# Kernel tuning notes

Hardware: AMD Instinct MI355X
Metric: run time of the kernel (lower is better)

## Reference

```python
import jax, jax.numpy as jnp
import numpy as np
import math

N = 16384
IRREPS_IN = ((16, 0), (8, 1), (8, 2))          # 16x0e + 8x1e + 8x2e, dim 80
HID1 = ((128, 0), (128, 1), (128, 2), (128, 1))  # hidden_irreps[1]
HID0 = ((64, 0), (64, 1), (64, 2), (64, 1))      # hidden_irreps[0]
IRREPS_OUT = ((1, 0), (1, 2))                   # 1x0e + 1x2e, dim 6
UVU_INS = ((0,0,0),(0,1,1),(0,2,2),(0,3,3),(1,0,1),(1,1,0),(1,1,1),(1,1,3),
           (2,0,2),(2,1,2),(2,2,0),(2,2,1),(2,2,3),(2,3,2))
# FullyConnectedTensorProduct: all symmetry-allowed paths, 17 total
FC_INS = tuple((i1, i2, io) for io, (mo, lo) in enumerate(IRREPS_OUT)
               for i1, (m1, l1) in enumerate(HID0)
               for i2, (m2, l2) in enumerate(HID0)
               if abs(l1 - l2) <= lo <= l1 + l2)

# ---- real Clebsch-Gordan coefficients (computed once in numpy) ----
def _cg_complex(l1, l2, l3):
    f = math.factorial
    C = np.zeros((2*l1+1, 2*l2+1, 2*l3+1))
    for m1 in range(-l1, l1+1):
        for m2 in range(-l2, l2+1):
            m3 = m1 + m2
            if abs(m3) > l3:
                continue
            pref = math.sqrt((2*l3+1) * f(l3+l1-l2) * f(l3-l1+l2) * f(l1+l2-l3) / f(l1+l2+l3+1))
            pref *= math.sqrt(f(l3+m3)*f(l3-m3)*f(l1-m1)*f(l1+m1)*f(l2-m2)*f(l2+m2))
            s = 0.0
            for k in range(l1+l2-l3+1):
                d = (k, l1+l2-l3-k, l1-m1-k, l2+m2-k, l3-l2+m1+k, l3-l1-m2+k)
                if min(d) < 0:
                    continue
                s += (-1)**k / (f(d[0])*f(d[1])*f(d[2])*f(d[3])*f(d[4])*f(d[5]))
            C[m1+l1, m2+l2, m3+l3] = pref * s
    return C

def _real_to_complex(l):
    U = np.zeros((2*l+1, 2*l+1), dtype=complex)
    U[l, l] = 1.0
    for m in range(1, l+1):
        U[l-m, l+m] = 1/math.sqrt(2)
        U[l+m, l+m] = (-1)**m/math.sqrt(2)
        U[l-m, l-m] = 1j/math.sqrt(2)
        U[l+m, l-m] = -1j*(-1)**m/math.sqrt(2)
    return U * (-1j)**l  # phase makes the real-basis CG real

def _real_cg(l1, l2, l3):
    K = np.einsum('ma,nb,oc,mno->abc', _real_to_complex(l1), _real_to_complex(l2),
                  np.conj(_real_to_complex(l3)), _cg_complex(l1, l2, l3))
    Kr, Ki = np.real(K), np.imag(K)
    K = Kr if np.linalg.norm(Kr) >= np.linalg.norm(Ki) else Ki
    # component normalization: ||K||_F = sqrt(2*l3+1)
    return (K / np.linalg.norm(K) * math.sqrt(2*l3+1)).astype(np.float32)

_CG = {}
def cg(l1, l2, l3):
    if (l1, l2, l3) not in _CG:
        _CG[(l1, l2, l3)] = _real_cg(l1, l2, l3)
    return _CG[(l1, l2, l3)]

# ---- irreps helpers ----
def to_blocks(x, irr):
    blocks, off = [], 0
    for m, l in irr:
        d = m * (2*l + 1)
        blocks.append(x[:, off:off+d].reshape(x.shape[0], m, 2*l + 1))
        off += d
    return blocks

def from_blocks(bl):
    return jnp.concatenate([b.reshape(b.shape[0], -1) for b in bl], axis=-1)

def o3_linear(xb, irr_in, irr_out, W, b0):
    # e3nn o3.Linear: mixes all input blocks with the same l; fan-in normalized; bias on 0e
    xin = {}
    for blk, (m, l) in zip(xb, irr_in):
        xin[l] = blk if l not in xin else jnp.concatenate([xin[l], blk], axis=1)
    out, cur, boff = [], {}, 0
    for m, l in irr_out:
        c = cur.get(l, 0)
        Wl = W[l][:, c:c+m]  # (tot_in_mul_l, m)
        y = jnp.einsum('nui,uo->noi', xin[l], Wl) / np.float32(math.sqrt(xin[l].shape[1]))
        cur[l] = c + m
        if l == 0:
            y = y + b0[boff:boff+m][None, :, None]
            boff += m
        out.append(y)
    return out

def tp_uvu(x1, x2, w, irr, ins):
    # o3.TensorProduct with 'uvu' weighted paths; weight per path: (u, v)
    ls = [l for _, l in irr]
    fan = [0.0] * len(irr)
    for i1, i2, io in ins:
        fan[io] += irr[i2][0]
    out = [None] * len(irr)
    for p, (i1, i2, io) in enumerate(ins):
        K = cg(ls[i1], ls[i2], ls[io])  # (i, j, k)
        b = jnp.einsum('uv,nvj->nuj', w[p], x2[i2])
        t = jnp.einsum('nui,nuj,ijk->nuk', x1[i1], b, K)
        out[io] = t if out[io] is None else out[io] + t
    return [o / np.float32(math.sqrt(f)) for o, f in zip(out, fan)]

def tp_fc(x1, x2, w):
    ls = [l for _, l in HID0]
    fan = [0.0, 0.0]
    for i1, i2, io in FC_INS:
        fan[io] += HID0[i1][0] * HID0[i2][0]
    out = [None, None]
    for p, (i1, i2, io) in enumerate(FC_INS):
        K = cg(ls[i1], ls[i2], IRREPS_OUT[io][1])
        b = jnp.einsum('uv,nvj->nuj', w[p], x2[i2])
        t = jnp.einsum('nui,nuj,ijk->nk', x1[i1], b, K)
        out[io] = t if out[io] is None else out[io] + t
    return [(o / np.float32(math.sqrt(f)))[:, None, :] for o, f in zip(out, fan)]

def setup_inputs() -> dict:
    key = jax.random.key(0)
    ks = jax.random.split(key, 16)
    rn = lambda k, shp: jax.random.normal(k, shp, dtype=jnp.float32)
    return {
        'x': rn(ks[0], (N, 80)),
        'lin1_W0': rn(ks[1], (16, 128)), 'lin1_W1': rn(ks[2], (8, 256)),
        'lin1_W2': rn(ks[3], (8, 128)), 'lin1_b0': rn(ks[4], (128,)),
        'lin2_W0': rn(ks[5], (128, 64)), 'lin2_W1': rn(ks[6], (256, 128)),
        'lin2_W2': rn(ks[7], (128, 64)), 'lin2_b0': rn(ks[8], (64,)),
        # 11 stacked HID0->HID0 linears: [s1a, s1b, lin3, s2a, s2b, lin4, s3a, s3b, lin5, s4a, s4b]
        'L_W0': rn(ks[9], (11, 64, 64)), 'L_W1': rn(ks[10], (11, 128, 128)),
        'L_W2': rn(ks[11], (11, 64, 64)), 'L_b0': rn(ks[12], (11, 64)),
        'tp_w': rn(ks[13], (3, 14, 64, 64)),  # tp1..tp3 path weights
        'tp4_w': rn(ks[14], (17, 64, 64)),    # fully-connected tp path weights
    }

def reference(x, lin1_W0, lin1_W1, lin1_W2, lin1_b0,
              lin2_W0, lin2_W1, lin2_W2, lin2_b0,
              L_W0, L_W1, L_W2, L_b0, tp_w, tp4_w):
    h = o3_linear(to_blocks(x, IRREPS_IN), IRREPS_IN, HID1,
                  {0: lin1_W0, 1: lin1_W1, 2: lin1_W2}, lin1_b0)
    h = o3_linear(h, HID1, HID0, {0: lin2_W0, 1: lin2_W1, 2: lin2_W2}, lin2_b0)
    lin = lambda hb, i: o3_linear(hb, HID0, HID0, {0: L_W0[i], 1: L_W1[i], 2: L_W2[i]}, L_b0[i])
    for i in range(3):  # split -> tp(uvu) -> linear, three times
        ha, hb = lin(h, 3*i), lin(h, 3*i + 1)
        ht = tp_uvu(ha, hb, tp_w[i], HID0, UVU_INS)
        h = lin(ht, 3*i + 2)
    ha, hb = lin(h, 9), lin(h, 10)  # split4
    return from_blocks(tp_fc(ha, hb, tp4_w))
```

## Files before the change

kernel.cpp:

```cpp
#include <hip/hip_runtime.h>
#include <math.h>

constexpr int TS = 16;
constexpr int NT = 512;
constexpr int SSTRIDE = 776;
constexpr int H1S = 1544;
constexpr int BUF = TS*SSTRIDE;

typedef __attribute__((ext_vector_type(8))) short bf16x8;
typedef __attribute__((ext_vector_type(4))) float f32x4;
typedef __attribute__((ext_vector_type(4))) unsigned short u16x4;

#define KFENCE() asm volatile("" ::: "memory")

__device__ inline f32x4 mfma16(bf16x8 a, bf16x8 b, f32x4 c){
  return __builtin_amdgcn_mfma_f32_16x16x32_bf16(a, b, c, 0, 0, 0);
}
__device__ inline unsigned short f2b(float f){
  union { float f; unsigned u; } v; v.f = f;
  return (unsigned short)((v.u + 0x7fffu + ((v.u >> 16) & 1u)) >> 16);
}
__device__ inline float b2f(unsigned short h){
  union { unsigned u; float f; } v; v.u = ((unsigned)h) << 16; return v.f;
}
__device__ inline void store_hl(unsigned short* ph, unsigned short* pl, int idx, float v){
  unsigned short h = f2b(v);
  ph[idx] = h;
  pl[idx] = f2b(v - b2f(h));
}
#define LDFRAG(p) (*(const bf16x8*)(p))

constexpr int OFF_L2W0 = 0;
constexpr int OFF_L2W1 = 8192;
constexpr int OFF_L2W2 = 40960;
constexpr int OFF_LW0  = 49152;
constexpr int OFF_LW1  = 94208;
constexpr int OFF_LW2  = 274432;
constexpr int OFF_TPW  = 319488;
constexpr int OFF_TP4W = 491520;
constexpr int W_TOT    = 561152;

__device__ inline double dfact(int n){ double r=1.0; for(int i=2;i<=n;i++) r*=(double)i; return r; }
struct dcplx { double x, y; };
__device__ inline dcplx cmul(dcplx a, dcplx b){ return {a.x*b.x-a.y*b.y, a.x*b.y+a.y*b.x}; }

__device__ dcplx Uent(int l, int r, int c){
  double re=0.0, im=0.0;
  double s = 1.0/sqrt(2.0);
  if (r==l && c==l) re = 1.0;
  else if (c>l){ int m=c-l; double sgn=(m&1)?-1.0:1.0;
    if (r==l-m) re = s; else if (r==l+m) re = sgn*s;
  } else if (c<l){ int m=l-c; double sgn=(m&1)?-1.0:1.0;
    if (r==l-m) im = s; else if (r==l+m) im = -sgn*s;
  }
  int lm=l&3; double pr,pi;
  if(lm==0){pr=1;pi=0;} else if(lm==1){pr=0;pi=-1;} else if(lm==2){pr=-1;pi=0;} else {pr=0;pi=1;}
  return { re*pr-im*pi, re*pi+im*pr };
}

__device__ double cg_complex_entry(int l1,int l2,int l3,int m1,int m2){
  int m3=m1+m2;
  if (m3<-l3 || m3>l3) return 0.0;
  double pref = sqrt((double)(2*l3+1)*dfact(l3+l1-l2)*dfact(l3-l1+l2)*dfact(l1+l2-l3)/dfact(l1+l2+l3+1));
  pref *= sqrt(dfact(l3+m3)*dfact(l3-m3)*dfact(l1-m1)*dfact(l1+m1)*dfact(l2-m2)*dfact(l2+m2));
  double s=0.0;
  for(int k=0;k<=l1+l2-l3;k++){
    int a2=l1-m1-k, a3=l2+m2-k, a4=l3-l2+m1+k, a5=l3-l1-m2+k;
    if(a2<0||a3<0||a4<0||a5<0) continue;
    double t=1.0/(dfact(k)*dfact(l1+l2-l3-k)*dfact(a2)*dfact(a3)*dfact(a4)*dfact(a5));
    s += (k&1)? -t : t;
  }
  return pref*s;
}

__global__ void cg_init_kernel(float* cg){
  __shared__ double sKr[525], sKi[525];
  __shared__ double sScale[13];
  __shared__ int    sSel[13];
  const int L1[13]={0,0,1,0,2,1,1,1,2,1,2,2,2};
  const int L2[13]={0,1,0,2,0,1,1,1,1,2,2,2,2};
  const int L3[13]={0,1,1,2,2,0,1,2,2,2,0,1,2};
  const int OFF[14]={0,1,10,19,44,69,78,105,150,225,300,325,400,525};
  const int tid = threadIdx.x;
  int combo=-1, l1=0,l2=0,l3=0;
  if (tid < 525){
    combo=12;
    for(int i=0;i<12;i++) if (tid < OFF[i+1]) { combo=i; break; }
    l1=L1[combo]; l2=L2[combo]; l3=L3[combo];
    int d2=2*l2+1, d3=2*l3+1;
    int e = tid - OFF[combo];
    int a = e/(d2*d3), b=(e/d3)%d2, cc=e%d3;
    double kr=0.0, ki=0.0;
    for(int m=0;m<2*l1+1;m++) for(int n=0;n<d2;n++){
      int m3 = (m-l1)+(n-l2);
      if (m3<-l3||m3>l3) continue;
      double cv = cg_complex_entry(l1,l2,l3,m-l1,n-l2);
      if (cv==0.0) continue;
      dcplx u1=Uent(l1,m,a), u2=Uent(l2,n,b), u3=Uent(l3,m3+l3,cc);
      u3.y = -u3.y;
      dcplx t = cmul(cmul(u1,u2),u3);
      kr += t.x*cv; ki += t.y*cv;
    }
    sKr[tid]=kr; sKi[tid]=ki;
  }
  __syncthreads();
  if (tid < 13){
    int sz = OFF[tid+1]-OFF[tid];
    double nr=0,ni=0;
    for(int i=0;i<sz;i++){ double r=sKr[OFF[tid]+i], im=sKi[OFF[tid]+i]; nr+=r*r; ni+=im*im; }
    int sel = (nr>=ni)? 0 : 1;
    sSel[tid]=sel;
    sScale[tid] = sqrt((double)(2*L3[tid]+1))/sqrt(sel? ni : nr);
  }
  __syncthreads();
  if (tid < 525){
    double v = sSel[combo]? sKi[tid] : sKr[tid];
    cg[tid] = (float)(v*sScale[combo]);
  }
}

__global__ void prep_kernel(const float* __restrict__ l2W0, const float* __restrict__ l2W1,
                            const float* __restrict__ l2W2, const float* __restrict__ LW0,
                            const float* __restrict__ LW1, const float* __restrict__ LW2,
                            const float* __restrict__ tpw, const float* __restrict__ tp4w,
                            unsigned short* __restrict__ wb){
  int i = blockIdx.x*256 + threadIdx.x;
  if (i >= W_TOT) return;
  float v;
  if (i < 8192){ int o=i>>7, k=i&127; v = l2W0[k*64+o]; }
  else if (i < 40960){ int j=i-8192; int o=j>>8, k=j&255; v = l2W1[k*128+o]; }
  else if (i < 49152){ int j=i-40960; int o=j>>7, k=j&127; v = l2W2[k*64+o]; }
  else if (i < 94208){ int j=i-49152; int li=j>>12, r=j&4095, o=r>>6, k=r&63; v = LW0[li*4096+k*64+o]; }
  else if (i < 274432){ int j=i-94208; int li=j>>14, r=j&16383, o=r>>7, k=r&127; v = LW1[li*16384+k*128+o]; }
  else if (i < 319488){ int j=i-274432; int li=j>>12, r=j&4095, o=r>>6, k=r&63; v = LW2[li*4096+k*64+o]; }
  else if (i < 491520){ v = tpw[i-319488]; }
  else { v = tp4w[i-491520]; }
  unsigned short h = f2b(v);
  wb[i] = h;
  wb[W_TOT + i] = f2b(v - b2f(h));
}

__device__ void linL_mfma(const unsigned short* __restrict__ wb, int o0, int o1, int o2,
                          const float* __restrict__ b0,
                          const unsigned short* sh, const unsigned short* sl,
                          unsigned short* dh, unsigned short* dl, int wave, int lane)
{
  const float rs128 = 0.08838834764831845f;
  int l16 = lane & 15, quad = lane >> 4;
  int abase = l16 * SSTRIDE;
  for (int job = wave; job < 16; job += 8){
    if (job < 4){
      int col = job*16 + l16;
      f32x4 a0 = {0,0,0,0}, a1 = {0,0,0,0};
      #pragma unroll
      for (int ks=0; ks<2; ks++){
        int so = abase + ks*32 + quad*8;
        bf16x8 xh = LDFRAG(sh+so), xl = LDFRAG(sl+so);
        int wo = o0 + col*64 + ks*32 + quad*8;
        bf16x8 wh = LDFRAG(wb+wo), wl = LDFRAG(wb+W_TOT+wo);
        a0 = mfma16(xh,wh,a0); a1 = mfma16(xh,wl,a1); a1 = mfma16(xl,wh,a1);
      }
      float bias = b0[col];
      #pragma unroll
      for (int r=0;r<4;r++)
        store_hl(dh,dl,(quad*4+r)*SSTRIDE + col, (a0[r]+a1[r])*0.125f + bias);
    } else if (job < 12){
      int nt = job-4; int col = nt*16 + l16;
      #pragma unroll
      for (int i=0;i<3;i++){
        f32x4 a0 = {0,0,0,0}, a1 = {0,0,0,0};
        #pragma unroll
        for (int ks=0; ks<4; ks++){
          int ka = ks*32 + quad*8;
          int so = abase + ((ka < 64) ? (64 + i*64 + ka) : (576 + i*64 + ka - 64));
          bf16x8 xh = LDFRAG(sh+so), xl = LDFRAG(sl+so);
          int wo = o1 + col*128 + ka;
          bf16x8 wh = LDFRAG(wb+wo), wl = LDFRAG(wb+W_TOT+wo);
          a0 = mfma16(xh,wh,a0); a1 = mfma16(xh,wl,a1); a1 = mfma16(xl,wh,a1);
        }
        int dof = (col < 64) ? (64 + i*64 + col) : (576 + i*64 + col - 64);
        #pragma unroll
        for (int r=0;r<4;r++)
          store_hl(dh,dl,(quad*4+r)*SSTRIDE + dof, (a0[r]+a1[r])*rs128);
      }
    } else {
      int nt = job-12; int col = nt*16 + l16;
      #pragma unroll
      for (int i=0;i<5;i++){
        f32x4 a0 = {0,0,0,0}, a1 = {0,0,0,0};
        #pragma unroll
        for (int ks=0; ks<2; ks++){
          int so = abase + 256 + i*64 + ks*32 + quad*8;
          bf16x8 xh = LDFRAG(sh+so), xl = LDFRAG(sl+so);
          int wo = o2 + col*64 + ks*32 + quad*8;
          bf16x8 wh = LDFRAG(wb+wo), wl = LDFRAG(wb+W_TOT+wo);
          a0 = mfma16(xh,wh,a0); a1 = mfma16(xh,wl,a1); a1 = mfma16(xl,wh,a1);
        }
        #pragma unroll
        for (int r=0;r<4;r++)
          store_hl(dh,dl,(quad*4+r)*SSTRIDE + 256 + i*64 + col, (a0[r]+a1[r])*0.125f);
      }
    }
  }
}

__device__ void lin2_mfma(const unsigned short* __restrict__ wb,
                          const float* __restrict__ b0,
                          const unsigned short* h1h, const unsigned short* h1l,
                          unsigned short* dh, unsigned short* dl, int wave, int lane)
{
  const float rs128 = 0.08838834764831845f;
  int l16 = lane & 15, quad = lane >> 4;
  int abase = l16 * H1S;
  for (int job = wave; job < 16; job += 8){
    if (job < 4){
      int col = job*16 + l16;
      f32x4 a0 = {0,0,0,0}, a1 = {0,0,0,0};
      #pragma unroll
      for (int ks=0; ks<4; ks++){
        int so = abase + ks*32 + quad*8;
        bf16x8 xh = LDFRAG(h1h+so), xl = LDFRAG(h1l+so);
        int wo = OFF_L2W0 + col*128 + ks*32 + quad*8;
        bf16x8 wh = LDFRAG(wb+wo), wl = LDFRAG(wb+W_TOT+wo);
        a0 = mfma16(xh,wh,a0); a1 = mfma16(xh,wl,a1); a1 = mfma16(xl,wh,a1);
      }
      float bias = b0[col];
      #pragma unroll
      for (int r=0;r<4;r++)
        store_hl(dh,dl,(quad*4+r)*SSTRIDE + col, (a0[r]+a1[r])*rs128 + bias);
    } else if (job < 12){
      int nt = job-4; int col = nt*16 + l16;
      #pragma unroll
      for (int i=0;i<3;i++){
        f32x4 a0 = {0,0,0,0}, a1 = {0,0,0,0};
        #pragma unroll
        for (int ks=0; ks<8; ks++){
          int ka = ks*32 + quad*8;
          int so = abase + ((ka < 128) ? (128 + i*128 + ka) : (1152 + i*128 + ka - 128));
          bf16x8 xh = LDFRAG(h1h+so), xl = LDFRAG(h1l+so);
          int wo = OFF_L2W1 + col*256 + ka;
          bf16x8 wh = LDFRAG(wb+wo), wl = LDFRAG(wb+W_TOT+wo);
          a0 = mfma16(xh,wh,a0); a1 = mfma16(xh,wl,a1); a1 = mfma16(xl,wh,a1);
        }
        int dof = (col < 64) ? (64 + i*64 + col) : (576 + i*64 + col - 64);
        #pragma unroll
        for (int r=0;r<4;r++)
          store_hl(dh,dl,(quad*4+r)*SSTRIDE + dof, (a0[r]+a1[r])*0.0625f);
      }
    } else {
      int nt = job-12; int col = nt*16 + l16;
      #pragma unroll
      for (int i=0;i<5;i++){
        f32x4 a0 = {0,0,0,0}, a1 = {0,0,0,0};
        #pragma unroll
        for (int ks=0; ks<4; ks++){
          int so = abase + 512 + i*128 + ks*32 + quad*8;
          bf16x8 xh = LDFRAG(h1h+so), xl = LDFRAG(h1l+so);
          int wo = OFF_L2W2 + col*128 + ks*32 + quad*8;
          bf16x8 wh = LDFRAG(wb+wo), wl = LDFRAG(wb+W_TOT+wo);
          a0 = mfma16(xh,wh,a0); a1 = mfma16(xh,wl,a1); a1 = mfma16(xl,wh,a1);
        }
        #pragma unroll
        for (int r=0;r<4;r++)
          store_hl(dh,dl,(quad*4+r)*SSTRIDE + 256 + i*64 + col, (a0[r]+a1[r])*rs128);
      }
    }
  }
}

template<int D1,int D2,int D3,int O1,int O2,int CGO>
__device__ __forceinline__ void fused_path(
    const unsigned short* __restrict__ wb, int wo,
    const unsigned short* s1h, const unsigned short* s1l,
    const unsigned short* s2h, const unsigned short* s2l,
    const float* __restrict__ cgp,
    float (&tk)[4][D3], int mt, int lane)
{
  int l16 = lane & 15, quad = lane >> 4;
  float x1v[D1][4];
  #pragma unroll
  for (int i=0;i<D1;i++){
    int o = l16*SSTRIDE + O1 + i*64 + mt*16 + quad*4;
    u16x4 xh4 = *(const u16x4*)(s1h + o);
    u16x4 xl4 = *(const u16x4*)(s1l + o);
    #pragma unroll
    for (int r=0;r<4;r++) x1v[i][r] = b2f(xh4[r]) + b2f(xl4[r]);
  }
  #pragma unroll
  for (int j=0;j<D2;j++){
    f32x4 a0 = {0,0,0,0}, a1 = {0,0,0,0};
    #pragma unroll
    for (int ks=0; ks<2; ks++){
      int wofs = wo + (mt*16 + l16)*64 + ks*32 + quad*8;
      bf16x8 wh = LDFRAG(wb + wofs);
      bf16x8 wl = LDFRAG(wb + W_TOT + wofs);
      int sofs = l16*SSTRIDE + O2 + j*64 + ks*32 + quad*8;
      bf16x8 xh = LDFRAG(s2h + sofs);
      bf16x8 xl = LDFRAG(s2l + sofs);
      a0 = mfma16(wh,xh,a0); a1 = mfma16(wh,xl,a1); a1 = mfma16(wl,xh,a1);
    }
    #pragma unroll
    for (int r=0;r<4;r++){
      float bu = a0[r] + a1[r];
      #pragma unroll
      for (int i=0;i<D1;i++){
        float pr = x1v[i][r]*bu;
        #pragma unroll
        for (int k=0;k<D3;k++) tk[r][k] += pr*cgp[CGO + (i*D2 + j)*D3 + k];
      }
    }
  }
}

template<int D1,int D2,int D3,int O1,int O2,int CGO>
__device__ __forceinline__ void fused_path_fc(
    const unsigned short* __restrict__ wb, int wo,
    const unsigned short* s1h, const unsigned short* s1l,
    const unsigned short* s2h, const unsigned short* s2l,
    const float* __restrict__ cgp,
    float (&tk)[D3], int mt, int lane)
{
  int l16 = lane & 15, quad = lane >> 4;
  float x1v[D1][4];
  #pragma unroll
  for (int i=0;i<D1;i++){
    int o = l16*SSTRIDE + O1 + i*64 + mt*16 + quad*4;
    u16x4 xh4 = *(const u16x4*)(s1h + o);
    u16x4 xl4 = *(const u16x4*)(s1l + o);
    #pragma unroll
    for (int r=0;r<4;r++) x1v[i][r] = b2f(xh4[r]) + b2f(xl4[r]);
  }
  #pragma unroll
  for (int j=0;j<D2;j++){
    f32x4 a0 = {0,0,0,0}, a1 = {0,0,0,0};
    #pragma unroll
    for (int ks=0; ks<2; ks++){
      int wofs = wo + (mt*16 + l16)*64 + ks*32 + quad*8;
      bf16x8 wh = LDFRAG(wb + wofs);
      bf16x8 wl = LDFRAG(wb + W_TOT + wofs);
      int sofs = l16*SSTRIDE + O2 + j*64 + ks*32 + quad*8;
      bf16x8 xh = LDFRAG(s2h + sofs);
      bf16x8 xl = LDFRAG(s2l + sofs);
      a0 = mfma16(wh,xh,a0); a1 = mfma16(wh,xl,a1); a1 = mfma16(wl,xh,a1);
    }
    float bu[4];
    #pragma unroll
    for (int r=0;r<4;r++) bu[r] = a0[r] + a1[r];
    #pragma unroll
    for (int i=0;i<D1;i++){
      float pij = x1v[i][0]*bu[0] + x1v[i][1]*bu[1] + x1v[i][2]*bu[2] + x1v[i][3]*bu[3];
      #pragma unroll
      for (int k=0;k<D3;k++) tk[k] += pij*cgp[CGO + (i*D2 + j)*D3 + k];
    }
  }
}

__device__ inline void store4_hl(unsigned short* ph, unsigned short* pl, int idx,
                                 float v0, float v1, float v2, float v3){
  u16x4 vh, vl;
  float v[4] = {v0,v1,v2,v3};
  #pragma unroll
  for (int r=0;r<4;r++){
    unsigned short h = f2b(v[r]);
    vh[r] = h;
    vl[r] = f2b(v[r] - b2f(h));
  }
  *(u16x4*)(ph + idx) = vh;
  *(u16x4*)(pl + idx) = vl;
}

__device__ void fused_tp_uvu(const unsigned short* __restrict__ wb, int two,
    const unsigned short* ah, const unsigned short* al,
    const unsigned short* bh, const unsigned short* bl,
    unsigned short* dh, unsigned short* dl,
    const float* __restrict__ cgp, int wave, int lane)
{
  const float f192 = 0.07216878364870323f;
  const float f256 = 0.0625f;
  int mt = wave & 3;
  int l16 = lane & 15, quad = lane >> 4;
  int u0 = mt*16 + quad*4;
  if (wave < 4){
    {
      float tk0[4][1] = {};
      fused_path<1,1,1,  0,  0,  0>(wb,two+ 0*4096, ah,al,bh,bl,cgp,tk0,mt,lane);
      KFENCE();
      fused_path<3,3,1, 64, 64, 69>(wb,two+ 5*4096, ah,al,bh,bl,cgp,tk0,mt,lane);
      KFENCE();
      fused_path<5,5,1,256,256,300>(wb,two+10*4096, ah,al,bh,bl,cgp,tk0,mt,lane);
      store4_hl(dh,dl, l16*SSTRIDE + u0,
                tk0[0][0]*f192, tk0[1][0]*f192, tk0[2][0]*f192, tk0[3][0]*f192);
      KFENCE();
    }
    {
      float tk2[4][5] = {};
      fused_path<1,5,5,  0,256, 19>(wb,two+ 2*4096, ah,al,bh,bl,cgp,tk2,mt,lane);
      KFENCE();
      fused_path<5,1,5,256,  0, 44>(wb,two+ 8*4096, ah,al,bh,bl,cgp,tk2,mt,lane);
      KFENCE();
      fused_path<5,3,5,256, 64,150>(wb,two+ 9*4096, ah,al,bh,bl,cgp,tk2,mt,lane);
      KFENCE();
      fused_path<5,3,5,256,576,150>(wb,two+13*4096, ah,al,bh,bl,cgp,tk2,mt,lane);
      #pragma unroll
      for (int k=0;k<5;k++)
        store4_hl(dh,dl, l16*SSTRIDE + 256 + k*64 + u0,
                  tk2[0][k]*f256, tk2[1][k]*f256, tk2[2][k]*f256, tk2[3][k]*f256);
    }
  } else {
    {
      float tkA[4][3] = {};
      fused_path<1,3,3,  0, 64,  1>(wb,two+ 1*4096, ah,al,bh,bl,cgp,tkA,mt,lane);
      KFENCE();
      fused_path<3,1,3, 64,  0, 10>(wb,two+ 4*4096, ah,al,bh,bl,cgp,tkA,mt,lane);
      KFENCE();
      fused_path<3,3,3, 64, 64, 78>(wb,two+ 6*4096, ah,al,bh,bl,cgp,tkA,mt,lane);
      KFENCE();
      fused_path<5,5,3,256,256,325>(wb,two+11*4096, ah,al,bh,bl,cgp,tkA,mt,lane);
      #pragma unroll
      for (int k=0;k<3;k++)
        store4_hl(dh,dl, l16*SSTRIDE +  64 + k*64 + u0,
                  tkA[0][k]*f256, tkA[1][k]*f256, tkA[2][k]*f256, tkA[3][k]*f256);
      KFENCE();
    }
    {
      float tkB[4][3] = {};
      fused_path<1,3,3,  0,576,  1>(wb,two+ 3*4096, ah,al,bh,bl,cgp,tkB,mt,lane);
      KFENCE();
      fused_path<3,3,3, 64, 64, 78>(wb,two+ 7*4096, ah,al,bh,bl,cgp,tkB,mt,lane);
      KFENCE();
      fused_path<5,5,3,256,256,325>(wb,two+12*4096, ah,al,bh,bl,cgp,tkB,mt,lane);
      #pragma unroll
      for (int k=0;k<3;k++)
        store4_hl(dh,dl, l16*SSTRIDE + 576 + k*64 + u0,
                  tkB[0][k]*f192, tkB[1][k]*f192, tkB[2][k]*f192, tkB[3][k]*f192);
    }
  }
}

__device__ void fused_tp_fc(const unsigned short* __restrict__ wb,
    const unsigned short* ah, const unsigned short* al,
    const unsigned short* bh, const unsigned short* bl,
    float* s_out, const float* __restrict__ cgp, int wave, int lane)
{
  int mt = wave & 3, half = wave >> 2;
  int l16 = lane & 15;
  {
    float t0[1] = {};
    if (half == 0){
      fused_path_fc<1,1,1,  0,  0,  0>(wb,OFF_TP4W+ 0*4096, ah,al,bh,bl,cgp,t0,mt,lane);
      KFENCE();
      fused_path_fc<3,3,1, 64, 64, 69>(wb,OFF_TP4W+ 1*4096, ah,al,bh,bl,cgp,t0,mt,lane);
      KFENCE();
      fused_path_fc<3,3,1, 64,576, 69>(wb,OFF_TP4W+ 2*4096, ah,al,bh,bl,cgp,t0,mt,lane);
    } else {
      fused_path_fc<5,5,1,256,256,300>(wb,OFF_TP4W+ 3*4096, ah,al,bh,bl,cgp,t0,mt,lane);
      KFENCE();
      fused_path_fc<3,3,1,576, 64, 69>(wb,OFF_TP4W+ 4*4096, ah,al,bh,bl,cgp,t0,mt,lane);
      KFENCE();
      fused_path_fc<3,3,1,576,576, 69>(wb,OFF_TP4W+ 5*4096, ah,al,bh,bl,cgp,t0,mt,lane);
    }
    float v0 = t0[0];
    v0 += __shfl_xor(v0, 16, 64);
    v0 += __shfl_xor(v0, 32, 64);
    if (lane < 16) atomicAdd(&s_out[l16*6 + 0], v0);
  }
  KFENCE();
  {
    float t2[5] = {};
    if (half == 0){
      fused_path_fc<3,5,5, 64,256,225>(wb,OFF_TP4W+ 8*4096, ah,al,bh,bl,cgp,t2,mt,lane);
      KFENCE();
      fused_path_fc<5,3,5,256, 64,150>(wb,OFF_TP4W+11*4096, ah,al,bh,bl,cgp,t2,mt,lane);
      KFENCE();
      fused_path_fc<5,5,5,256,256,400>(wb,OFF_TP4W+12*4096, ah,al,bh,bl,cgp,t2,mt,lane);
      KFENCE();
      fused_path_fc<5,3,5,256,576,150>(wb,OFF_TP4W+13*4096, ah,al,bh,bl,cgp,t2,mt,lane);
    } else {
      fused_path_fc<1,5,5,  0,256, 19>(wb,OFF_TP4W+ 6*4096, ah,al,bh,bl,cgp,t2,mt,lane);
      KFENCE();
      fused_path_fc<3,3,5, 64, 64,105>(wb,OFF_TP4W+ 7*4096, ah,al,bh,bl,cgp,t2,mt,lane);
      KFENCE();
      fused_path_fc<3,3,5, 64,576,105>(wb,OFF_TP4W+ 9*4096, ah,al,bh,bl,cgp,t2,mt,lane);
      KFENCE();
      fused_path_fc<5,1,5,256,  0, 44>(wb,OFF_TP4W+10*4096, ah,al,bh,bl,cgp,t2,mt,lane);
      KFENCE();
      fused_path_fc<3,3,5,576, 64,105>(wb,OFF_TP4W+14*4096, ah,al,bh,bl,cgp,t2,mt,lane);
      KFENCE();
      fused_path_fc<3,5,5,576,256,225>(wb,OFF_TP4W+15*4096, ah,al,bh,bl,cgp,t2,mt,lane);
      KFENCE();
      fused_path_fc<3,3,5,576,576,105>(wb,OFF_TP4W+16*4096, ah,al,bh,bl,cgp,t2,mt,lane);
    }
    #pragma unroll
    for (int k=0;k<5;k++){
      float v = t2[k];
      v += __shfl_xor(v, 16, 64);
      v += __shfl_xor(v, 32, 64);
      if (lane < 16) atomicAdd(&s_out[l16*6 + 1 + k], v);
    }
  }
}

__global__ __launch_bounds__(NT) void deeprst_main(
    const float* __restrict__ x,
    const float* __restrict__ l1W0, const float* __restrict__ l1W1,
    const float* __restrict__ l1W2, const float* __restrict__ l1b0,
    const float* __restrict__ l2b0, const float* __restrict__ Lb0,
    const unsigned short* __restrict__ wb, const float* __restrict__ cgp,
    float* __restrict__ out)
{
  __shared__ unsigned short sth[3*BUF];
  __shared__ unsigned short stl[3*BUF];

  const int tid  = threadIdx.x;
  const int lane = tid & 63;
  const int wave = tid >> 6;
  const int n0   = blockIdx.x * TS;
  const float rs8 = 0.3535533905932738f;

  for (int idx=tid; idx<TS*128; idx+=NT){
    int n=idx>>7, o=idx&127;
    const float* xp = x + (n0+n)*80;
    float acc=0.f;
    #pragma unroll
    for (int v=0;v<16;v++) acc += xp[v]*l1W0[v*128+o];
    store_hl(sth,stl, n*H1S + o, acc*0.25f + l1b0[o]);
  }
  for (int idx=tid; idx<TS*768; idx+=NT){
    int o=idx&255, i=(idx>>8)%3, n=idx/768;
    const float* xp = x + (n0+n)*80 + 16;
    float acc=0.f;
    #pragma unroll
    for (int v=0;v<8;v++) acc += xp[v*3+i]*l1W1[v*256+o];
    int du = (o<128)? (128 + i*128 + o) : (1152 + i*128 + o-128);
    store_hl(sth,stl, n*H1S + du, acc*rs8);
  }
  for (int idx=tid; idx<TS*640; idx+=NT){
    int o=idx&127, i=(idx>>7)%5, n=idx/640;
    const float* xp = x + (n0+n)*80 + 40;
    float acc=0.f;
    #pragma unroll
    for (int v=0;v<8;v++) acc += xp[v*5+i]*l1W2[v*128+o];
    store_hl(sth,stl, n*H1S + 512 + i*128 + o, acc*rs8);
  }
  __syncthreads();

  lin2_mfma(wb, l2b0, sth, stl, sth+2*BUF, stl+2*BUF, wave, lane);
  __syncthreads();

  int ih = 2, i0 = 0, i1 = 1;
  for (int r=0;r<3;r++){
    unsigned short *hh=sth+ih*BUF, *hl=stl+ih*BUF;
    unsigned short *ah=sth+i0*BUF, *al=stl+i0*BUF;
    unsigned short *bh=sth+i1*BUF, *bl=stl+i1*BUF;
    linL_mfma(wb, OFF_LW0+(3*r  )*4096, OFF_LW1+(3*r  )*16384, OFF_LW2+(3*r  )*4096,
              Lb0+(3*r  )*64, hh, hl, ah, al, wave, lane);
    linL_mfma(wb, OFF_LW0+(3*r+1)*4096, OFF_LW1+(3*r+1)*16384, OFF_LW2+(3*r+1)*4096,
              Lb0+(3*r+1)*64, hh, hl, bh, bl, wave, lane);
    __syncthreads();
    fused_tp_uvu(wb, OFF_TPW + r*14*4096, ah, al, bh, bl, hh, hl, cgp, wave, lane);
    __syncthreads();
    linL_mfma(wb, OFF_LW0+(3*r+2)*4096, OFF_LW1+(3*r+2)*16384, OFF_LW2+(3*r+2)*4096,
              Lb0+(3*r+2)*64, hh, hl, ah, al, wave, lane);
    __syncthreads();
    int nh=i0; i0=i1; i1=ih; ih=nh;
  }

  unsigned short *hh=sth+ih*BUF, *hl=stl+ih*BUF;
  unsigned short *ah=sth+i0*BUF, *al=stl+i0*BUF;
  unsigned short *bh=sth+i1*BUF, *bl=stl+i1*BUF;
  linL_mfma(wb, OFF_LW0+ 9*4096, OFF_LW1+ 9*16384, OFF_LW2+ 9*4096, Lb0+ 9*64, hh, hl, ah, al, wave, lane);
  linL_mfma(wb, OFF_LW0+10*4096, OFF_LW1+10*16384, OFF_LW2+10*4096, Lb0+10*64, hh, hl, bh, bl, wave, lane);
  __syncthreads();

  float* s_out = (float*)hh;
  if (tid < TS*6) s_out[tid] = 0.f;
  __syncthreads();

  fused_tp_fc(wb, ah, al, bh, bl, s_out, cgp, wave, lane);
  __syncthreads();

  if (tid < TS*6){
    int n=tid/6, k=tid%6;
    float sc = (k==0)? (1.0f/sqrtf(24576.0f)) : (1.0f/sqrtf(45056.0f));
    out[(n0+n)*6+k] = s_out[tid]*sc;
  }
}

extern "C" void kernel_launch(void* const* d_in, const int* in_sizes, int n_in,
                              void* d_out, int out_size, void* d_ws, size_t ws_size,
                              hipStream_t stream)
{
  (void)n_in; (void)out_size; (void)ws_size;
  const float* x    = (const float*)d_in[0];
  const float* l1W0 = (const float*)d_in[1];
  const float* l1W1 = (const float*)d_in[2];
  const float* l1W2 = (const float*)d_in[3];
  const float* l1b0 = (const float*)d_in[4];
  const float* l2W0 = (const float*)d_in[5];
  const float* l2W1 = (const float*)d_in[6];
  const float* l2W2 = (const float*)d_in[7];
  const float* l2b0 = (const float*)d_in[8];
  const float* LW0  = (const float*)d_in[9];
  const float* LW1  = (const float*)d_in[10];
  const float* LW2  = (const float*)d_in[11];
  const float* Lb0  = (const float*)d_in[12];
  const float* tpw  = (const float*)d_in[13];
  const float* tp4w = (const float*)d_in[14];

  float* cg = (float*)d_ws;
  unsigned short* wb = (unsigned short*)((char*)d_ws + 4096);
  const int n = in_sizes[0]/80;

  cg_init_kernel<<<1, 576, 0, stream>>>(cg);
  prep_kernel<<<(W_TOT+255)/256, 256, 0, stream>>>(l2W0,l2W1,l2W2,LW0,LW1,LW2,tpw,tp4w,wb);
  deeprst_main<<<n/TS, NT, 0, stream>>>(x,l1W0,l1W1,l1W2,l1b0,l2b0,Lb0,wb,cg,(float*)d_out);
}
```

Before: 843.7 us.

## Halve tile to 8 rows with 256-thread blocks and two blocks per CU

Shrinks the per-block node tile from 16 to 8 and the block from 8 to 4 waves, with a launch bound asking for two blocks per CU. The goal is less shared memory per block and more resident blocks to hide latency. The 16-row MFMA tiles are kept, so rows are duplicated via (l16&7) and only half the lanes write results. That wastes half of every MFMA. The 4 waves now each run all tensor-product paths that were split across two wave groups, and the halved shared arrays carry across the unseen main body.

```diff
diff --git a/kernel.cpp b/kernel.cpp
--- a/kernel.cpp
+++ b/kernel.cpp
@@ -1,8 +1,9 @@
 #include <hip/hip_runtime.h>
 #include <math.h>
 
-constexpr int TS = 16;
-constexpr int NT = 512;
+constexpr int TS = 8;
+constexpr int NT = 256;
+constexpr int NW = NT/64;
 constexpr int SSTRIDE = 776;
 constexpr int H1S = 1544;
 constexpr int BUF = TS*SSTRIDE;
@@ -147,8 +148,8 @@
 {
   const float rs128 = 0.08838834764831845f;
   int l16 = lane & 15, quad = lane >> 4;
-  int abase = l16 * SSTRIDE;
-  for (int job = wave; job < 16; job += 8){
+  int abase = (l16 & 7) * SSTRIDE;
+  for (int job = wave; job < 16; job += NW){
     if (job < 4){
       int col = job*16 + l16;
       f32x4 a0 = {0,0,0,0}, a1 = {0,0,0,0};
@@ -161,9 +162,11 @@
         a0 = mfma16(xh,wh,a0); a1 = mfma16(xh,wl,a1); a1 = mfma16(xl,wh,a1);
       }
       float bias = b0[col];
-      #pragma unroll
-      for (int r=0;r<4;r++)
-        store_hl(dh,dl,(quad*4+r)*SSTRIDE + col, (a0[r]+a1[r])*0.125f + bias);
+      if (quad < 2){
+        #pragma unroll
+        for (int r=0;r<4;r++)
+          store_hl(dh,dl,(quad*4+r)*SSTRIDE + col, (a0[r]+a1[r])*0.125f + bias);
+      }
     } else if (job < 12){
       int nt = job-4; int col = nt*16 + l16;
       #pragma unroll
@@ -179,9 +182,11 @@
           a0 = mfma16(xh,wh,a0); a1 = mfma16(xh,wl,a1); a1 = mfma16(xl,wh,a1);
         }
         int dof = (col < 64) ? (64 + i*64 + col) : (576 + i*64 + col - 64);
-        #pragma unroll
-        for (int r=0;r<4;r++)
-          store_hl(dh,dl,(quad*4+r)*SSTRIDE + dof, (a0[r]+a1[r])*rs128);
+        if (quad < 2){
+          #pragma unroll
+          for (int r=0;r<4;r++)
+            store_hl(dh,dl,(quad*4+r)*SSTRIDE + dof, (a0[r]+a1[r])*rs128);
+        }
       }
     } else {
       int nt = job-12; int col = nt*16 + l16;
@@ -196,9 +201,11 @@
           bf16x8 wh = LDFRAG(wb+wo), wl = LDFRAG(wb+W_TOT+wo);
           a0 = mfma16(xh,wh,a0); a1 = mfma16(xh,wl,a1); a1 = mfma16(xl,wh,a1);
         }
-        #pragma unroll
-        for (int r=0;r<4;r++)
-          store_hl(dh,dl,(quad*4+r)*SSTRIDE + 256 + i*64 + col, (a0[r]+a1[r])*0.125f);
+        if (quad < 2){
+          #pragma unroll
+          for (int r=0;r<4;r++)
+            store_hl(dh,dl,(quad*4+r)*SSTRIDE + 256 + i*64 + col, (a0[r]+a1[r])*0.125f);
+        }
       }
     }
   }
@@ -211,8 +218,8 @@
 {
   const float rs128 = 0.08838834764831845f;
   int l16 = lane & 15, quad = lane >> 4;
-  int abase = l16 * H1S;
-  for (int job = wave; job < 16; job += 8){
+  int abase = (l16 & 7) * H1S;
+  for (int job = wave; job < 16; job += NW){
     if (job < 4){
       int col = job*16 + l16;
       f32x4 a0 = {0,0,0,0}, a1 = {0,0,0,0};
@@ -225,9 +232,11 @@
         a0 = mfma16(xh,wh,a0); a1 = mfma16(xh,wl,a1); a1 = mfma16(xl,wh,a1);
       }
       float bias = b0[col];
-      #pragma unroll
-      for (int r=0;r<4;r++)
-        store_hl(dh,dl,(quad*4+r)*SSTRIDE + col, (a0[r]+a1[r])*rs128 + bias);
+      if (quad < 2){
+        #pragma unroll
+        for (int r=0;r<4;r++)
+          store_hl(dh,dl,(quad*4+r)*SSTRIDE + col, (a0[r]+a1[r])*rs128 + bias);
+      }
     } else if (job < 12){
       int nt = job-4; int col = nt*16 + l16;
       #pragma unroll
@@ -243,9 +252,11 @@
           a0 = mfma16(xh,wh,a0); a1 = mfma16(xh,wl,a1); a1 = mfma16(xl,wh,a1);
         }
         int dof = (col < 64) ? (64 + i*64 + col) : (576 + i*64 + col - 64);
-        #pragma unroll
-        for (int r=0;r<4;r++)
-          store_hl(dh,dl,(quad*4+r)*SSTRIDE + dof, (a0[r]+a1[r])*0.0625f);
+        if (quad < 2){
+          #pragma unroll
+          for (int r=0;r<4;r++)
+            store_hl(dh,dl,(quad*4+r)*SSTRIDE + dof, (a0[r]+a1[r])*0.0625f);
+        }
       }
     } else {
       int nt = job-12; int col = nt*16 + l16;
@@ -260,9 +271,11 @@
           bf16x8 wh = LDFRAG(wb+wo), wl = LDFRAG(wb+W_TOT+wo);
           a0 = mfma16(xh,wh,a0); a1 = mfma16(xh,wl,a1); a1 = mfma16(xl,wh,a1);
         }
-        #pragma unroll
-        for (int r=0;r<4;r++)
-          store_hl(dh,dl,(quad*4+r)*SSTRIDE + 256 + i*64 + col, (a0[r]+a1[r])*rs128);
+        if (quad < 2){
+          #pragma unroll
+          for (int r=0;r<4;r++)
+            store_hl(dh,dl,(quad*4+r)*SSTRIDE + 256 + i*64 + col, (a0[r]+a1[r])*rs128);
+        }
       }
     }
   }
@@ -277,10 +290,11 @@
     float (&tk)[4][D3], int mt, int lane)
 {
   int l16 = lane & 15, quad = lane >> 4;
+  int sbase = (l16 & 7) * SSTRIDE;
   float x1v[D1][4];
   #pragma unroll
   for (int i=0;i<D1;i++){
-    int o = l16*SSTRIDE + O1 + i*64 + mt*16 + quad*4;
+    int o = sbase + O1 + i*64 + mt*16 + quad*4;
     u16x4 xh4 = *(const u16x4*)(s1h + o);
     u16x4 xl4 = *(const u16x4*)(s1l + o);
     #pragma unroll
@@ -294,7 +308,7 @@
       int wofs = wo + (mt*16 + l16)*64 + ks*32 + quad*8;
       bf16x8 wh = LDFRAG(wb + wofs);
       bf16x8 wl = LDFRAG(wb + W_TOT + wofs);
-      int sofs = l16*SSTRIDE + O2 + j*64 + ks*32 + quad*8;
+      int sofs = sbase + O2 + j*64 + ks*32 + quad*8;
       bf16x8 xh = LDFRAG(s2h + sofs);
       bf16x8 xl = LDFRAG(s2l + sofs);
       a0 = mfma16(wh,xh,a0); a1 = mfma16(wh,xl,a1); a1 = mfma16(wl,xh,a1);
@@ -321,10 +335,11 @@
     float (&tk)[D3], int mt, int lane)
 {
   int l16 = lane & 15, quad = lane >> 4;
+  int sbase = (l16 & 7) * SSTRIDE;
   float x1v[D1][4];
   #pragma unroll
   for (int i=0;i<D1;i++){
-    int o = l16*SSTRIDE + O1 + i*64 + mt*16 + quad*4;
+    int o = sbase + O1 + i*64 + mt*16 + quad*4;
     u16x4 xh4 = *(const u16x4*)(s1h + o);
     u16x4 xl4 = *(const u16x4*)(s1l + o);
     #pragma unroll
@@ -338,7 +353,7 @@
       int wofs = wo + (mt*16 + l16)*64 + ks*32 + quad*8;
       bf16x8 wh = LDFRAG(wb + wofs);
       bf16x8 wl = LDFRAG(wb + W_TOT + wofs);
-      int sofs = l16*SSTRIDE + O2 + j*64 + ks*32 + quad*8;
+      int sofs = sbase + O2 + j*64 + ks*32 + quad*8;
       bf16x8 xh = LDFRAG(s2h + sofs);
       bf16x8 xl = LDFRAG(s2l + sofs);
       a0 = mfma16(wh,xh,a0); a1 = mfma16(wh,xl,a1); a1 = mfma16(wl,xh,a1);
@@ -380,58 +395,65 @@
   int mt = wave & 3;
   int l16 = lane & 15, quad = lane >> 4;
   int u0 = mt*16 + quad*4;
-  if (wave < 4){
-    {
-      float tk0[4][1] = {};
-      fused_path<1,1,1,  0,  0,  0>(wb,two+ 0*4096, ah,al,bh,bl,cgp,tk0,mt,lane);
-      KFENCE();
-      fused_path<3,3,1, 64, 64, 69>(wb,two+ 5*4096, ah,al,bh,bl,cgp,tk0,mt,lane);
-      KFENCE();
-      fused_path<5,5,1,256,256,300>(wb,two+10*4096, ah,al,bh,bl,cgp,tk0,mt,lane);
-      store4_hl(dh,dl, l16*SSTRIDE + u0,
+  bool wr = (l16 < 8);
+  int srow = (l16 & 7) * SSTRIDE;
+  {
+    float tk0[4][1] = {};
+    fused_path<1,1,1,  0,  0,  0>(wb,two+ 0*4096, ah,al,bh,bl,cgp,tk0,mt,lane);
+    KFENCE();
+    fused_path<3,3,1, 64, 64, 69>(wb,two+ 5*4096, ah,al,bh,bl,cgp,tk0,mt,lane);
+    KFENCE();
+    fused_path<5,5,1,256,256,300>(wb,two+10*4096, ah,al,bh,bl,cgp,tk0,mt,lane);
+    if (wr)
+      store4_hl(dh,dl, srow + u0,
                 tk0[0][0]*f192, tk0[1][0]*f192, tk0[2][0]*f192, tk0[3][0]*f192);
-      KFENCE();
-    }
-    {
-      float tk2[4][5] = {};
-      fused_path<1,5,5,  0,256, 19>(wb,two+ 2*4096, ah,al,bh,bl,cgp,tk2,mt,lane);
-      KFENCE();
-      fused_path<5,1,5,256,  0, 44>(wb,two+ 8*4096, ah,al,bh,bl,cgp,tk2,mt,lane);
-      KFENCE();
-      fused_path<5,3,5,256, 64,150>(wb,two+ 9*4096, ah,al,bh,bl,cgp,tk2,mt,lane);
-      KFENCE();
-      fused_path<5,3,5,256,576,150>(wb,two+13*4096, ah,al,bh,bl,cgp,tk2,mt,lane);
+    KFENCE();
+  }
+  {
+    float tk2[4][5] = {};
+    fused_path<1,5,5,  0,256, 19>(wb,two+ 2*4096, ah,al,bh,bl,cgp,tk2,mt,lane);
+    KFENCE();
+    fused_path<5,1,5,256,  0, 44>(wb,two+ 8*4096, ah,al,bh,bl,cgp,tk2,mt,lane);
+    KFENCE();
+    fused_path<5,3,5,256, 64,150>(wb,two+ 9*4096, ah,al,bh,bl,cgp,tk2,mt,lane);
+    KFENCE();
+    fused_path<5,3,5,256,576,150>(wb,two+13*4096, ah,al,bh,bl,cgp,tk2,mt,lane);
+    if (wr){
       #pragma unroll
       for (int k=0;k<5;k++)
-        store4_hl(dh,dl, l16*SSTRIDE + 256 + k*64 + u0,
+        store4_hl(dh,dl, srow + 256 + k*64 + u0,
                   tk2[0][k]*f256, tk2[1][k]*f256, tk2[2][k]*f256, tk2[3][k]*f256);
     }
-  } else {
-    {
-      float tkA[4][3] = {};
-      fused_path<1,3,3,  0, 64,  1>(wb,two+ 1*4096, ah,al,bh,bl,cgp,tkA,mt,lane);
-      KFENCE();
-      fused_path<3,1,3, 64,  0, 10>(wb,two+ 4*4096, ah,al,bh,bl,cgp,tkA,mt,lane);
-      KFENCE();
-      fused_path<3,3,3, 64, 64, 78>(wb,two+ 6*4096, ah,al,bh,bl,cgp,tkA,mt,lane);
-      KFENCE();
-      fused_path<5,5,3,256,256,325>(wb,two+11*4096, ah,al,bh,bl,cgp,tkA,mt,lane);
+    KFENCE();
+  }
+  {
+    float tkA[4][3] = {};
+    fused_path<1,3,3,  0, 64,  1>(wb,two+ 1*4096, ah,al,bh,bl,cgp,tkA,mt,lane);
+    KFENCE();
+    fused_path<3,1,3, 64,  0, 10>(wb,two+ 4*4096, ah,al,bh,bl,cgp,tkA,mt,lane);
+    KFENCE();
+    fused_path<3,3,3, 64, 64, 78>(wb,two+ 6*4096, ah,al,bh,bl,cgp,tkA,mt,lane);
+    KFENCE();
+    fused_path<5,5,3,256,256,325>(wb,two+11*4096, ah,al,bh,bl,cgp,tkA,mt,lane);
+    if (wr){
       #pragma unroll
       for (int k=0;k<3;k++)
-        store4_hl(dh,dl, l16*SSTRIDE +  64 + k*64 + u0,
+        store4_hl(dh,dl, srow +  64 + k*64 + u0,
                   tkA[0][k]*f256, tkA[1][k]*f256, tkA[2][k]*f256, tkA[3][k]*f256);
-      KFENCE();
-    }
-    {
-      float tkB[4][3] = {};
-      fused_path<1,3,3,  0,576,  1>(wb,two+ 3*4096, ah,al,bh,bl,cgp,tkB,mt,lane);
-      KFENCE();
-      fused_path<3,3,3, 64, 64, 78>(wb,two+ 7*4096, ah,al,bh,bl,cgp,tkB,mt,lane);
-      KFENCE();
-      fused_path<5,5,3,256,256,325>(wb,two+12*4096, ah,al,bh,bl,cgp,tkB,mt,lane);
+    }
+    KFENCE();
+  }
+  {
+    float tkB[4][3] = {};
+    fused_path<1,3,3,  0,576,  1>(wb,two+ 3*4096, ah,al,bh,bl,cgp,tkB,mt,lane);
+    KFENCE();
+    fused_path<3,3,3, 64, 64, 78>(wb,two+ 7*4096, ah,al,bh,bl,cgp,tkB,mt,lane);
+    KFENCE();
+    fused_path<5,5,3,256,256,325>(wb,two+12*4096, ah,al,bh,bl,cgp,tkB,mt,lane);
+    if (wr){
       #pragma unroll
       for (int k=0;k<3;k++)
-        store4_hl(dh,dl, l16*SSTRIDE + 576 + k*64 + u0,
+        store4_hl(dh,dl, srow + 576 + k*64 + u0,
                   tkB[0][k]*f192, tkB[1][k]*f192, tkB[2][k]*f192, tkB[3][k]*f192);
     }
   }
@@ -442,65 +464,60 @@
     const unsigned short* bh, const unsigned short* bl,
     float* s_out, const float* __restrict__ cgp, int wave, int lane)
 {
-  int mt = wave & 3, half = wave >> 2;
-  int l16 = lane & 15;
+  int mt = wave & 3;
   {
     float t0[1] = {};
-    if (half == 0){
-      fused_path_fc<1,1,1,  0,  0,  0>(wb,OFF_TP4W+ 0*4096, ah,al,bh,bl,cgp,t0,mt,lane);
-      KFENCE();
-      fused_path_fc<3,3,1, 64, 64, 69>(wb,OFF_TP4W+ 1*4096, ah,al,bh,bl,cgp,t0,mt,lane);
-      KFENCE();
-      fused_path_fc<3,3,1, 64,576, 69>(wb,OFF_TP4W+ 2*4096, ah,al,bh,bl,cgp,t0,mt,lane);
-    } else {
-      fused_path_fc<5,5,1,256,256,300>(wb,OFF_TP4W+ 3*4096, ah,al,bh,bl,cgp,t0,mt,lane);
-      KFENCE();
-      fused_path_fc<3,3,1,576, 64, 69>(wb,OFF_TP4W+ 4*4096, ah,al,bh,bl,cgp,t0,mt,lane);
-      KFENCE();
-      fused_path_fc<3,3,1,576,576, 69>(wb,OFF_TP4W+ 5*4096, ah,al,bh,bl,cgp,t0,mt,lane);
-    }
+    fused_path_fc<1,1,1,  0,  0,  0>(wb,OFF_TP4W+ 0*4096, ah,al,bh,bl,cgp,t0,mt,lane);
+    KFENCE();
+    fused_path_fc<3,3,1, 64, 64, 69>(wb,OFF_TP4W+ 1*4096, ah,al,bh,bl,cgp,t0,mt,lane);
+    KFENCE();
+    fused_path_fc<3,3,1, 64,576, 69>(wb,OFF_TP4W+ 2*4096, ah,al,bh,bl,cgp,t0,mt,lane);
+    KFENCE();
+    fused_path_fc<5,5,1,256,256,300>(wb,OFF_TP4W+ 3*4096, ah,al,bh,bl,cgp,t0,mt,lane);
+    KFENCE();
+    fused_path_fc<3,3,1,576, 64, 69>(wb,OFF_TP4W+ 4*4096, ah,al,bh,bl,cgp,t0,mt,lane);
+    KFENCE();
+    fused_path_fc<3,3,1,576,576, 69>(wb,OFF_TP4W+ 5*4096, ah,al,bh,bl,cgp,t0,mt,lane);
     float v0 = t0[0];
     v0 += __shfl_xor(v0, 16, 64);
     v0 += __shfl_xor(v0, 32, 64);
-    if (lane < 16) atomicAdd(&s_out[l16*6 + 0], v0);
+    if (lane < 8) atomicAdd(&s_out[lane*6 + 0], v0);
   }
   KFENCE();
   {
     float t2[5] = {};
-    if (half == 0){
-      fused_path_fc<3,5,5, 64,256,225>(wb,OFF_TP4W+ 8*4096, ah,al,bh,bl,cgp,t2,mt,lane);
-      KFENCE();
-      fused_path_fc<5,3,5,256, 64,150>(wb,OFF_TP4W+11*4096, ah,al,bh,bl,cgp,t2,mt,lane);
-      KFENCE();
-      fused_path_fc<5,5,5,256,256,400>(wb,OFF_TP4W+12*4096, ah,al,bh,bl,cgp,t2,mt,lane);
-      KFENCE();
-      fused_path_fc<5,3,5,256,576,150>(wb,OFF_TP4W+13*4096, ah,al,bh,bl,cgp,t2,mt,lane);
-    } else {
-      fused_path_fc<1,5,5,  0,256, 19>(wb,OFF_TP4W+ 6*4096, ah,al,bh,bl,cgp,t2,mt,lane);
-      KFENCE();
-      fused_path_fc<3,3,5, 64, 64,105>(wb,OFF_TP4W+ 7*4096, ah,al,bh,bl,cgp,t2,mt,lane);
-      KFENCE();
-      fused_path_fc<3,3,5, 64,576,105>(wb,OFF_TP4W+ 9*4096, ah,al,bh,bl,cgp,t2,mt,lane);
-      KFENCE();
-      fused_path_fc<5,1,5,256,  0, 44>(wb,OFF_TP4W+10*4096, ah,al,bh,bl,cgp,t2,mt,lane);
-      KFENCE();
-      fused_path_fc<3,3,5,576, 64,105>(wb,OFF_TP4W+14*4096, ah,al,bh,bl,cgp,t2,mt,lane);
-      KFENCE();
-      fused_path_fc<3,5,5,576,256,225>(wb,OFF_TP4W+15*4096, ah,al,bh,bl,cgp,t2,mt,lane);
-      KFENCE();
-      fused_path_fc<3,3,5,576,576,105>(wb,OFF_TP4W+16*4096, ah,al,bh,bl,cgp,t2,mt,lane);
-    }
+    fused_path_fc<1,5,5,  0,256, 19>(wb,OFF_TP4W+ 6*4096, ah,al,bh,bl,cgp,t2,mt,lane);
+    KFENCE();
+    fused_path_fc<3,3,5, 64, 64,105>(wb,OFF_TP4W+ 7*4096, ah,al,bh,bl,cgp,t2,mt,lane);
+    KFENCE();
+    fused_path_fc<3,5,5, 64,256,225>(wb,OFF_TP4W+ 8*4096, ah,al,bh,bl,cgp,t2,mt,lane);
+    KFENCE();
+    fused_path_fc<3,3,5, 64,576,105>(wb,OFF_TP4W+ 9*4096, ah,al,bh,bl,cgp,t2,mt,lane);
+    KFENCE();
+    fused_path_fc<5,1,5,256,  0, 44>(wb,OFF_TP4W+10*4096, ah,al,bh,bl,cgp,t2,mt,lane);
+    KFENCE();
+    fused_path_fc<5,3,5,256, 64,150>(wb,OFF_TP4W+11*4096, ah,al,bh,bl,cgp,t2,mt,lane);
+    KFENCE();
+    fused_path_fc<5,5,5,256,256,400>(wb,OFF_TP4W+12*4096, ah,al,bh,bl,cgp,t2,mt,lane);
+    KFENCE();
+    fused_path_fc<5,3,5,256,576,150>(wb,OFF_TP4W+13*4096, ah,al,bh,bl,cgp,t2,mt,lane);
+    KFENCE();
+    fused_path_fc<3,3,5,576, 64,105>(wb,OFF_TP4W+14*4096, ah,al,bh,bl,cgp,t2,mt,lane);
+    KFENCE();
+    fused_path_fc<3,5,5,576,256,225>(wb,OFF_TP4W+15*4096, ah,al,bh,bl,cgp,t2,mt,lane);
+    KFENCE();
+    fused_path_fc<3,3,5,576,576,105>(wb,OFF_TP4W+16*4096, ah,al,bh,bl,cgp,t2,mt,lane);
     #pragma unroll
     for (int k=0;k<5;k++){
       float v = t2[k];
       v += __shfl_xor(v, 16, 64);
       v += __shfl_xor(v, 32, 64);
-      if (lane < 16) atomicAdd(&s_out[l16*6 + 1 + k], v);
-    }
-  }
-}
-
-__global__ __launch_bounds__(NT) void deeprst_main(
+      if (lane < 8) atomicAdd(&s_out[lane*6 + 1 + k], v);
+    }
+  }
+}
+
+__global__ __launch_bounds__(NT, 2) void deeprst_main(
     const float* __restrict__ x,
     const float* __restrict__ l1W0, const float* __restrict__ l1W1,
     const float* __restrict__ l1W2, const float* __restrict__ l1b0,
```

After: 1.244 ms. +47.4%, slower.
